# Performance work log

Measured on AMD Instinct MI355X. Metric: run time of the kernel, lower is better.

The kernel has to match this reference:

```python
import jax, jax.numpy as jnp
import numpy as np

B, D, K, C = 512, 256, 65536, 1000
T_SUP, T_DC, LS = 0.07, 0.1, 0.1
EPS = 1e-8


def _l2norm(x, axis):
    return x / jnp.linalg.norm(x, axis=axis, keepdims=True)


def setup_inputs() -> dict:
    key = jax.random.key(0)
    k1, k2, k3, k4, k5, k6, k7, k8 = jax.random.split(key, 8)
    norm_q = _l2norm(jax.random.normal(k1, (B, D), jnp.float32), axis=1)
    k_feat = _l2norm(jax.random.normal(k2, (B, D), jnp.float32), axis=1)
    q_logits = jax.random.normal(k3, (B, C), jnp.float32)
    logits_k = jax.random.normal(k4, (B, C), jnp.float32)
    queue = _l2norm(jax.random.normal(k5, (D, K), jnp.float32), axis=0)
    # queue_label_prob stores softmaxed class-probabilities column-wise (prob.T)
    queue_label_prob = jax.nn.softmax(jax.random.normal(k6, (C, K), jnp.float32), axis=0)
    queue_label = jax.random.randint(k7, (K,), 0, C, jnp.int64)
    target = jax.random.randint(k8, (B,), 0, C, jnp.int64)
    return {
        "norm_q": norm_q, "q_logits": q_logits, "k_feat": k_feat,
        "logits_k": logits_k, "queue": queue,
        "queue_label_prob": queue_label_prob, "queue_label": queue_label,
        "target": target, "knn_k": 200,
    }


def reference(norm_q, q_logits, k_feat, logits_k, queue, queue_label_prob,
              queue_label, target, knn_k):
    b = norm_q.shape[0]

    # ---- supcon_in ----
    sim = norm_q @ queue                                  # [B, K]
    _, idx = jax.lax.top_k(sim, knn_k)                    # [B, knn_k]
    sim_knn = jnp.take_along_axis(sim, idx, axis=1)
    w = jax.nn.softmax(sim_knn / T_SUP, axis=-1)
    pos = (target[:, None] == queue_label[idx])           # [B, knn_k]
    gt = jnp.sum(w * pos, axis=1)                         # [B]
    m = gt > EPS
    supin_loss = jnp.sum(jnp.where(m, -jnp.log(jnp.where(m, gt, 1.0)), 0.0)) / b

    # ---- label-smoothed onehot ----
    onehot = jnp.full((b, C), LS / (C - 1), jnp.float32)
    onehot = onehot.at[jnp.arange(b), target].set(1.0 - LS)

    log_q = jax.nn.log_softmax(q_logits, axis=1)
    q_mask = jax.nn.softmax(q_logits, axis=1).min(axis=1) > EPS  # [B]

    # ---- fc loss (masked CE with label smoothing) ----
    fc_loss = -jnp.sum(jnp.sum(onehot * log_q, axis=1) * q_mask) / b

    # ---- generate_dc_target (no-grad in original) ----
    sim_k = jax.nn.softmax((k_feat @ queue) / T_DC, axis=-1)      # [B, K]
    dc_target = sim_k @ queue_label_prob.T                        # [B, C]

    # ---- dc loss: KL(dc_target || softmax(q_logits)), masked, sum / B ----
    kl = jnp.where(dc_target > 0, dc_target * (jnp.log(jnp.where(dc_target > 0, dc_target, 1.0)) - log_q), 0.0)
    dc_loss = jnp.sum(jnp.sum(kl, axis=1) * q_mask) / b

    return (supin_loss, fc_loss, dc_loss)
```

## Files before the change

### kernel.cpp

```cpp
#include <hip/hip_runtime.h>
#include <math.h>

#define BN 512
#define DN 256
#define KN 65536
#define CN 1000
#define EQ_CAP 512
#define EPSTR 136

typedef __attribute__((ext_vector_type(8))) short bf16x8;
typedef __attribute__((ext_vector_type(4))) float f32x4;

__device__ __forceinline__ unsigned short f2bf(float f) {
    unsigned u = __float_as_uint(f);
    unsigned r = (u + 0x7FFFu + ((u >> 16) & 1u)) >> 16;
    return (unsigned short)r;
}
__device__ __forceinline__ float bf2f(unsigned short h) {
    return __uint_as_float(((unsigned)h) << 16);
}
__device__ __forceinline__ unsigned fkey16(unsigned b) {
    b &= 0xFFFFu;
    return (b & 0x8000u) ? ((~b) & 0xFFFFu) : (b | 0x8000u);
}
__device__ __forceinline__ void async16(const void* g, void* l) {
    __builtin_amdgcn_global_load_lds(
        (const __attribute__((address_space(1))) unsigned*)g,
        (__attribute__((address_space(3))) unsigned*)l, 16, 0, 0);
}

__global__ void __launch_bounds__(256) cvt_bf16(const float* __restrict__ in,
                                                unsigned short* __restrict__ out) {
    int i = (blockIdx.x * 256 + threadIdx.x) * 4;
    float4 v = *(const float4*)&in[i];
    ushort4 o;
    o.x = f2bf(v.x); o.y = f2bf(v.y); o.z = f2bf(v.z); o.w = f2bf(v.w);
    *(ushort4*)&out[i] = o;
}

__global__ void __launch_bounds__(256) transpose_q(const float* __restrict__ Q,
                                                   unsigned short* __restrict__ Qt) {
    __shared__ float T[64][65];
    int tid = threadIdx.x;
    int n0 = blockIdx.x * 64;
    int d0 = blockIdx.y * 64;
    #pragma unroll
    for (int i = 0; i < 4; ++i) {
        int flat = i * 256 + tid;
        int d = flat >> 4, nq = (flat & 15) * 4;
        float4 v = *(const float4*)&Q[(size_t)(d0 + d) * KN + n0 + nq];
        T[d][nq] = v.x; T[d][nq + 1] = v.y; T[d][nq + 2] = v.z; T[d][nq + 3] = v.w;
    }
    __syncthreads();
    int n = tid >> 2, dbase = (tid & 3) * 16;
    unsigned u[8];
    #pragma unroll
    for (int j = 0; j < 8; ++j) {
        unsigned short a = f2bf(T[dbase + 2 * j][n]);
        unsigned short b = f2bf(T[dbase + 2 * j + 1][n]);
        u[j] = (unsigned)a | ((unsigned)b << 16);
    }
    unsigned short* o = &Qt[(size_t)(n0 + n) * DN + d0 + dbase];
    *(uint4*)o = make_uint4(u[0], u[1], u[2], u[3]);
    *(uint4*)(o + 8) = make_uint4(u[4], u[5], u[6], u[7]);
}

__global__ void __launch_bounds__(256) gemm_sim(const unsigned short* __restrict__ A,
                                                const unsigned short* __restrict__ Bt,
                                                unsigned short* __restrict__ simOut,
                                                unsigned short* __restrict__ expOut,
                                                float* __restrict__ Zb,
                                                int mBlockSplit) {
    __shared__ unsigned short smem[128 * 64 * 2];
    __shared__ float Zred[128];
    unsigned short* As = smem;
    unsigned short* Bs = smem + 128 * 64;
    int tid = threadIdx.x;
    int n0 = blockIdx.x * 128, m0 = blockIdx.y * 128;
    bool isExp = ((int)blockIdx.y >= mBlockSplit);
    int lane = tid & 63, w = tid >> 6;
    int l15 = lane & 15, quad = lane >> 4;
    int wm = w & 1, wn = w >> 1;
    f32x4 acc[4][4];
    #pragma unroll
    for (int mi = 0; mi < 4; ++mi)
        #pragma unroll
        for (int ni = 0; ni < 4; ++ni)
            #pragma unroll
            for (int j = 0; j < 4; ++j) acc[mi][ni][j] = 0.f;

    for (int k0 = 0; k0 < DN; k0 += 64) {
        #pragma unroll
        for (int i = 0; i < 4; ++i) {
            int f = (i * 256 + tid) * 8;
            async16(A + (size_t)(m0 + (f >> 6)) * DN + k0 + (f & 63), &As[f]);
        }
        #pragma unroll
        for (int i = 0; i < 4; ++i) {
            int f = (i * 256 + tid) * 8;
            async16(Bt + (size_t)(n0 + (f >> 6)) * DN + k0 + (f & 63), &Bs[f]);
        }
        __syncthreads();
        #pragma unroll
        for (int ks = 0; ks < 2; ++ks) {
            bf16x8 am[4], bn[4];
            #pragma unroll
            for (int mi = 0; mi < 4; ++mi)
                am[mi] = *(const bf16x8*)&As[(wm * 64 + mi * 16 + l15) * 64 + ks * 32 + quad * 8];
            #pragma unroll
            for (int ni = 0; ni < 4; ++ni)
                bn[ni] = *(const bf16x8*)&Bs[(wn * 64 + ni * 16 + l15) * 64 + ks * 32 + quad * 8];
            #pragma unroll
            for (int mi = 0; mi < 4; ++mi)
                #pragma unroll
                for (int ni = 0; ni < 4; ++ni)
                    acc[mi][ni] = __builtin_amdgcn_mfma_f32_16x16x32_bf16(bn[ni], am[mi], acc[mi][ni], 0, 0, 0);
        }
        __syncthreads();
    }

    unsigned short* obase = isExp ? expOut : simOut;
    int orow0 = isExp ? (m0 - mBlockSplit * 128) : m0;
    float rsum[4] = {0.f, 0.f, 0.f, 0.f};

    #pragma unroll
    for (int round = 0; round < 2; ++round) {
        if (wm == round) {
            #pragma unroll
            for (int mi = 0; mi < 4; ++mi) {
                int mrow = mi * 16 + l15;
                #pragma unroll
                for (int ni = 0; ni < 4; ++ni) {
                    int nc = wn * 64 + ni * 16 + quad * 4;
                    float v0 = acc[mi][ni][0], v1 = acc[mi][ni][1];
                    float v2 = acc[mi][ni][2], v3 = acc[mi][ni][3];
                    if (isExp) {
                        v0 = __expf(v0 * 10.0f); v1 = __expf(v1 * 10.0f);
                        v2 = __expf(v2 * 10.0f); v3 = __expf(v3 * 10.0f);
                    }
                    unsigned short u0 = f2bf(v0), u1 = f2bf(v1), u2 = f2bf(v2), u3 = f2bf(v3);
                    if (isExp) rsum[mi] += bf2f(u0) + bf2f(u1) + bf2f(u2) + bf2f(u3);
                    *(uint2*)&smem[mrow * EPSTR + nc] =
                        make_uint2((unsigned)u0 | ((unsigned)u1 << 16),
                                   (unsigned)u2 | ((unsigned)u3 << 16));
                }
            }
        }
        __syncthreads();
        #pragma unroll
        for (int j = 0; j < 4; ++j) {
            int fc = j * 256 + tid;
            int mr = fc >> 4;
            int ch = fc & 15;
            uint4 val = *(uint4*)&smem[mr * EPSTR + ch * 8];
            int g = orow0 + round * 64 + mr;
            *(uint4*)&obase[(size_t)g * KN + n0 + ch * 8] = val;
        }
        __syncthreads();
    }

    if (isExp) {
        float v4[4];
        #pragma unroll
        for (int mi = 0; mi < 4; ++mi) {
            float v = rsum[mi];
            v += __shfl_xor(v, 16, 64);
            v += __shfl_xor(v, 32, 64);
            v4[mi] = v;
        }
        if (wn == 0 && quad == 0) {
            #pragma unroll
            for (int mi = 0; mi < 4; ++mi) Zred[wm * 64 + mi * 16 + l15] = v4[mi];
        }
        __syncthreads();
        if (wn == 1 && quad == 0) {
            #pragma unroll
            for (int mi = 0; mi < 4; ++mi) Zred[wm * 64 + mi * 16 + l15] += v4[mi];
        }
        __syncthreads();
        if (tid < 128) atomicAdd(&Zb[orow0 + tid], Zred[tid]);
    }
}

__global__ void __launch_bounds__(256) supcon(const unsigned short* __restrict__ sim,
                                              const int* __restrict__ qlabel,
                                              const int* __restrict__ target,
                                              const int* __restrict__ knnp,
                                              float* __restrict__ out0) {
    __shared__ unsigned hist[4][256];
    __shared__ unsigned s_sel, s_cntAbove;
    __shared__ int eqIdx[EQ_CAP];
    __shared__ unsigned eqCount;
    __shared__ float redZ[256], redN[256];
    int tid = threadIdx.x, w = tid >> 6;
    int row = blockIdx.x;
    const unsigned short* srow = sim + (size_t)row * KN;
    int knn = *knnp;
    int tgt = target[row];
    if (tid == 0) { eqCount = 0u; }
    #pragma unroll
    for (int j = 0; j < 4; ++j) hist[j][tid] = 0u;
    __syncthreads();
    for (int i0 = tid * 4; i0 < KN; i0 += 1024) {
        uint2 v = *(const uint2*)&srow[i0];
        atomicAdd(&hist[w][fkey16(v.x) >> 8], 1u);
        atomicAdd(&hist[w][fkey16(v.x >> 16) >> 8], 1u);
        atomicAdd(&hist[w][fkey16(v.y) >> 8], 1u);
        atomicAdd(&hist[w][fkey16(v.y >> 16) >> 8], 1u);
    }
    __syncthreads();
    if (tid == 0) {
        unsigned acc = 0; int chosen = 0;
        for (int bin = 255; bin >= 0; --bin) {
            unsigned h = hist[0][bin] + hist[1][bin] + hist[2][bin] + hist[3][bin];
            if (acc + h >= (unsigned)knn) { chosen = bin; break; }
            acc += h;
        }
        s_cntAbove = acc; s_sel = (unsigned)chosen;
    }
    __syncthreads();
    unsigned selHi = s_sel;
    #pragma unroll
    for (int j = 0; j < 4; ++j) hist[j][tid] = 0u;
    __syncthreads();
    for (int i0 = tid * 4; i0 < KN; i0 += 1024) {
        uint2 v = *(const uint2*)&srow[i0];
        unsigned k0 = fkey16(v.x), k1 = fkey16(v.x >> 16), k2 = fkey16(v.y), k3 = fkey16(v.y >> 16);
        if ((k0 >> 8) == selHi) atomicAdd(&hist[w][k0 & 255u], 1u);
        if ((k1 >> 8) == selHi) atomicAdd(&hist[w][k1 & 255u], 1u);
        if ((k2 >> 8) == selHi) atomicAdd(&hist[w][k2 & 255u], 1u);
        if ((k3 >> 8) == selHi) atomicAdd(&hist[w][k3 & 255u], 1u);
    }
    __syncthreads();
    if (tid == 0) {
        unsigned acc = s_cntAbove; int chosen = 0;
        for (int bin = 255; bin >= 0; --bin) {
            unsigned h = hist[0][bin] + hist[1][bin] + hist[2][bin] + hist[3][bin];
            if (acc + h >= (unsigned)knn) { chosen = bin; break; }
            acc += h;
        }
        s_cntAbove = acc; s_sel = (selHi << 8) | (unsigned)chosen;
    }
    __syncthreads();
    unsigned tu = s_sel;
    unsigned cgt = s_cntAbove;
    const float invT = 1.0f / 0.07f;
    float Zl = 0.f, Nl = 0.f;
    for (int i0 = tid * 4; i0 < KN; i0 += 1024) {
        uint2 v = *(const uint2*)&srow[i0];
        unsigned bits[4] = {v.x & 0xFFFFu, v.x >> 16, v.y & 0xFFFFu, v.y >> 16};
        #pragma unroll
        for (int j = 0; j < 4; ++j) {
            unsigned u = fkey16(bits[j]);
            if (u > tu) {
                float e = __expf(bf2f((unsigned short)bits[j]) * invT);
                Zl += e;
                if (qlabel[i0 + j] == tgt) Nl += e;
            } else if (u == tu) {
                unsigned pos = atomicAdd(&eqCount, 1u);
                if (pos < EQ_CAP) eqIdx[pos] = i0 + j;
            }
        }
    }
    redZ[tid] = Zl; redN[tid] = Nl;
    __syncthreads();
    for (int s = 128; s > 0; s >>= 1) {
        if (tid < s) { redZ[tid] += redZ[tid + s]; redN[tid] += redN[tid + s]; }
        __syncthreads();
    }
    if (tid == 0) {
        float Z = redZ[0], num = redN[0];
        int neq = (int)(eqCount < (unsigned)EQ_CAP ? eqCount : (unsigned)EQ_CAP);
        int needed = knn - (int)cgt;
        if (needed > neq) needed = neq;
        for (int a = 1; a < neq; ++a) {
            int v = eqIdx[a]; int b2 = a - 1;
            while (b2 >= 0 && eqIdx[b2] > v) { eqIdx[b2 + 1] = eqIdx[b2]; --b2; }
            eqIdx[b2 + 1] = v;
        }
        unsigned tb = (tu & 0x8000u) ? (tu & 0x7FFFu) : ((~tu) & 0xFFFFu);
        float wt = __expf(bf2f((unsigned short)tb) * invT);
        for (int a = 0; a < needed; ++a) {
            Z += wt;
            if (qlabel[eqIdx[a]] == tgt) num += wt;
        }
        float gt = num / Z;
        if (gt > 1e-8f) atomicAdd(out0, -logf(gt) * (1.0f / (float)BN));
    }
}

__global__ void __launch_bounds__(256) dc_gemm(const unsigned short* __restrict__ E,
                                               const float* __restrict__ P,
                                               float* __restrict__ dct) {
    __shared__ unsigned short As[128 * 32];
    __shared__ unsigned short Bs[128 * 32];
    int tid = threadIdx.x;
    int c0 = blockIdx.x * 128, m0 = blockIdx.y * 128;
    int kb = blockIdx.z * (KN / 16);
    int lane = tid & 63, w = tid >> 6;
    int l15 = lane & 15, quad = lane >> 4;
    int wm = w & 1, wn = w >> 1;
    int crow = tid >> 1, khalf = (tid & 1) * 16;
    bool cvalid = (c0 + crow) < CN;
    const float* pbase = P + (size_t)(c0 + crow) * KN + khalf;
    f32x4 acc[4][4];
    #pragma unroll
    for (int r = 0; r < 4; ++r)
        #pragma unroll
        for (int c = 0; c < 4; ++c)
            #pragma unroll
            for (int j = 0; j < 4; ++j) acc[r][c][j] = 0.f;
    for (int kc = 0; kc < KN / 16; kc += 32) {
        int k0 = kb + kc;
        #pragma unroll
        for (int i = 0; i < 2; ++i) {
            int flat = (i * 256 + tid) * 8;
            int row = flat >> 5, kk = flat & 31;
            async16(E + (size_t)(m0 + row) * KN + k0 + kk, &As[flat]);
        }
        float4 p0 = make_float4(0.f, 0.f, 0.f, 0.f), p1 = p0, p2 = p0, p3 = p0;
        if (cvalid) {
            p0 = *(const float4*)&pbase[k0];
            p1 = *(const float4*)&pbase[k0 + 4];
            p2 = *(const float4*)&pbase[k0 + 8];
            p3 = *(const float4*)&pbase[k0 + 12];
        }
        unsigned u0 = (unsigned)f2bf(p0.x) | ((unsigned)f2bf(p0.y) << 16);
        unsigned u1 = (unsigned)f2bf(p0.z) | ((unsigned)f2bf(p0.w) << 16);
        unsigned u2 = (unsigned)f2bf(p1.x) | ((unsigned)f2bf(p1.y) << 16);
        unsigned u3 = (unsigned)f2bf(p1.z) | ((unsigned)f2bf(p1.w) << 16);
        unsigned u4 = (unsigned)f2bf(p2.x) | ((unsigned)f2bf(p2.y) << 16);
        unsigned u5 = (unsigned)f2bf(p2.z) | ((unsigned)f2bf(p2.w) << 16);
        unsigned u6 = (unsigned)f2bf(p3.x) | ((unsigned)f2bf(p3.y) << 16);
        unsigned u7 = (unsigned)f2bf(p3.z) | ((unsigned)f2bf(p3.w) << 16);
        *(uint4*)&Bs[crow * 32 + khalf] = make_uint4(u0, u1, u2, u3);
        *(uint4*)&Bs[crow * 32 + khalf + 8] = make_uint4(u4, u5, u6, u7);
        __syncthreads();
        bf16x8 af[4], bfr[4];
        #pragma unroll
        for (int r = 0; r < 4; ++r) af[r] = *(const bf16x8*)&As[(wm * 64 + r * 16 + l15) * 32 + quad * 8];
        #pragma unroll
        for (int c = 0; c < 4; ++c) bfr[c] = *(const bf16x8*)&Bs[(wn * 64 + c * 16 + l15) * 32 + quad * 8];
        #pragma unroll
        for (int r = 0; r < 4; ++r)
            #pragma unroll
            for (int c = 0; c < 4; ++c)
                acc[r][c] = __builtin_amdgcn_mfma_f32_16x16x32_bf16(af[r], bfr[c], acc[r][c], 0, 0, 0);
        __syncthreads();
    }
    #pragma unroll
    for (int r = 0; r < 4; ++r)
        #pragma unroll
        for (int reg = 0; reg < 4; ++reg) {
            int m = m0 + wm * 64 + r * 16 + quad * 4 + reg;
            #pragma unroll
            for (int c = 0; c < 4; ++c) {
                int cc = c0 + wn * 64 + c * 16 + l15;
                atomicAdd(&dct[m * 1024 + cc], acc[r][c][reg]);
            }
        }
}

__global__ void __launch_bounds__(256) logq_fc(const float* __restrict__ x_all,
                                               const int* __restrict__ target,
                                               float* __restrict__ logq,
                                               float* __restrict__ qmask,
                                               float* __restrict__ out1) {
    int row = blockIdx.x, tid = threadIdx.x;
    const float* x = x_all + (size_t)row * CN;
    __shared__ float red[256], red2[256];
    float mx = -INFINITY, mn = INFINITY;
    for (int c = tid; c < CN; c += 256) { float v = x[c]; mx = fmaxf(mx, v); mn = fminf(mn, v); }
    red[tid] = mx; red2[tid] = mn;
    __syncthreads();
    for (int s = 128; s > 0; s >>= 1) {
        if (tid < s) { red[tid] = fmaxf(red[tid], red[tid + s]); red2[tid] = fminf(red2[tid], red2[tid + s]); }
        __syncthreads();
    }
    mx = red[0]; mn = red2[0];
    __syncthreads();
    float se = 0.f, sx = 0.f;
    for (int c = tid; c < CN; c += 256) { float v = x[c]; se += __expf(v - mx); sx += v; }
    red[tid] = se; red2[tid] = sx;
    __syncthreads();
    for (int s = 128; s > 0; s >>= 1) {
        if (tid < s) { red[tid] += red[tid + s]; red2[tid] += red2[tid + s]; }
        __syncthreads();
    }
    float lse = mx + logf(red[0]);
    float sumlogq = red2[0] - (float)CN * lse;
    for (int c = tid; c < CN; c += 256) logq[(size_t)row * CN + c] = x[c] - lse;
    if (tid == 0) {
        float lqt = x[target[row]] - lse;
        bool qm = (mn - lse) > logf(1e-8f);
        qmask[row] = qm ? 1.0f : 0.0f;
        if (qm) {
            float fc = -(0.1f / 999.0f * (sumlogq - lqt) + 0.9f * lqt);
            atomicAdd(out1, fc * (1.0f / (float)BN));
        }
    }
}

__global__ void __launch_bounds__(256) dc_loss(const float* __restrict__ dct,
                                               const float* __restrict__ logq,
                                               const float* __restrict__ qmask,
                                               const float* __restrict__ Z,
                                               float* __restrict__ out2) {
    int row = blockIdx.x, tid = threadIdx.x;
    __shared__ float red[256];
    float invZ = 1.0f / Z[row];
    float s = 0.f;
    for (int c = tid; c < CN; c += 256) {
        float T = dct[row * 1024 + c] * invZ;
        if (T > 0.f) s += T * (logf(T) - logq[(size_t)row * CN + c]);
    }
    red[tid] = s;
    __syncthreads();
    for (int st = 128; st > 0; st >>= 1) {
        if (tid < st) red[tid] += red[tid + st];
        __syncthreads();
    }
    if (tid == 0 && qmask[row] > 0.f)
        atomicAdd(out2, red[0] * (1.0f / (float)BN));
}

extern "C" void kernel_launch(void* const* d_in, const int* in_sizes, int n_in,
                              void* d_out, int out_size, void* d_ws, size_t ws_size,
                              hipStream_t stream) {
    (void)in_sizes; (void)n_in; (void)out_size;
    const float* norm_q   = (const float*)d_in[0];
    const float* q_logits = (const float*)d_in[1];
    const float* k_feat   = (const float*)d_in[2];
    const float* queue    = (const float*)d_in[4];
    const float* qlp      = (const float*)d_in[5];
    const int*   qlabel   = (const int*)d_in[6];
    const int*   target   = (const int*)d_in[7];
    const int*   knnp     = (const int*)d_in[8];
    float* out = (float*)d_out;
    char* ws = (char*)d_ws;

    const size_t SIM_B = 67108864;
    const size_t QT_B  = 33554432;
    const size_t AC_B  = 524288;
    const size_t FUSED_NEED = SIM_B * 2 + QT_B + AC_B + 2097152 + 2048 + 2048000 + 2048;
    bool fused = (ws_size >= FUSED_NEED);

    unsigned short *simBF, *Ebf, *queueT, *Acat;
    float *dct, *Zb, *logq, *qmask;
    if (fused) {
        simBF  = (unsigned short*)(ws);
        Ebf    = (unsigned short*)(ws + SIM_B);
        queueT = (unsigned short*)(ws + 2 * SIM_B);
        Acat   = (unsigned short*)(ws + 2 * SIM_B + QT_B);
        dct    = (float*)(ws + 2 * SIM_B + QT_B + AC_B);
    } else {
        simBF  = (unsigned short*)(ws);
        Ebf    = simBF;
        queueT = (unsigned short*)(ws + SIM_B);
        Acat   = (unsigned short*)(ws + SIM_B + QT_B);
        dct    = (float*)(ws + SIM_B + QT_B + AC_B);
    }
    Zb    = (float*)((char*)dct + 2097152);
    logq  = (float*)((char*)Zb + 2048);
    qmask = (float*)((char*)logq + 2048000);

    hipMemsetAsync(dct, 0, 2097152 + 2048, stream);
    hipMemsetAsync(d_out, 0, 3 * sizeof(float), stream);

    cvt_bf16<<<dim3(128), 256, 0, stream>>>(norm_q, Acat);
    cvt_bf16<<<dim3(128), 256, 0, stream>>>(k_feat, Acat + (size_t)BN * DN);
    transpose_q<<<dim3(KN / 64, 4), 256, 0, stream>>>(queue, queueT);

    if (fused) {
        gemm_sim<<<dim3(KN / 128, 8), 256, 0, stream>>>(Acat, queueT, simBF, Ebf, Zb, 4);
        supcon<<<dim3(BN), 256, 0, stream>>>(simBF, qlabel, target, knnp, out + 0);
    } else {
        gemm_sim<<<dim3(KN / 128, 4), 256, 0, stream>>>(Acat, queueT, simBF, nullptr, nullptr, 4);
        supcon<<<dim3(BN), 256, 0, stream>>>(simBF, qlabel, target, knnp, out + 0);
        gemm_sim<<<dim3(KN / 128, 4), 256, 0, stream>>>(Acat + (size_t)BN * DN, queueT,
                                                        nullptr, Ebf, Zb, 0);
    }
    dc_gemm<<<dim3(8, 4, 16), 256, 0, stream>>>(Ebf, qlp, dct);
    logq_fc<<<dim3(BN), 256, 0, stream>>>(q_logits, target, logq, qmask, out + 1);
    dc_loss<<<dim3(BN), 256, 0, stream>>>(dct, logq, qmask, Zb, out + 2);
}
```

Measured before the change: 799.9 us.

## Widen dc_gemm K-tile to 64, swizzle LDS, double split-K, packed bf16 convert

The dc_gemm kernel now stages 64-wide K slices per iteration instead of 32, doing two MFMA k-steps per barrier pair. The B tile in LDS gets an XOR swizzle to avoid bank conflicts. The split-K factor goes from 16 to 32 so more blocks are in flight, with a launch-bounds occupancy hint of 3. The fp32-to-bf16 conversion of the probability matrix uses the hardware packed convert instruction. The aim is to cut barrier overhead and LDS conflicts and to better saturate bandwidth on the large fp32 P read. The cost is more LDS per block, and twice as many atomic adds into the output.

```diff
diff --git a/kernel.cpp b/kernel.cpp
--- a/kernel.cpp
+++ b/kernel.cpp
@@ -27,6 +27,11 @@
     __builtin_amdgcn_global_load_lds(
         (const __attribute__((address_space(1))) unsigned*)g,
         (__attribute__((address_space(3))) unsigned*)l, 16, 0, 0);
+}
+__device__ __forceinline__ unsigned cvtpk(float lo, float hi) {
+    unsigned r;
+    asm("v_cvt_pk_bf16_f32 %0, %1, %2" : "=v"(r) : "v"(lo), "v"(hi));
+    return r;
 }
 
 __global__ void __launch_bounds__(256) cvt_bf16(const float* __restrict__ in,
@@ -289,20 +294,21 @@
     }
 }
 
-__global__ void __launch_bounds__(256) dc_gemm(const unsigned short* __restrict__ E,
-                                               const float* __restrict__ P,
-                                               float* __restrict__ dct) {
-    __shared__ unsigned short As[128 * 32];
-    __shared__ unsigned short Bs[128 * 32];
+__global__ void __launch_bounds__(256, 3) dc_gemm(const unsigned short* __restrict__ E,
+                                                  const float* __restrict__ P,
+                                                  float* __restrict__ dct) {
+    __shared__ unsigned short As[128 * 64];
+    __shared__ unsigned short Bs[128 * 64];
     int tid = threadIdx.x;
     int c0 = blockIdx.x * 128, m0 = blockIdx.y * 128;
-    int kb = blockIdx.z * (KN / 16);
+    int kb = blockIdx.z * (KN / 32);
     int lane = tid & 63, w = tid >> 6;
     int l15 = lane & 15, quad = lane >> 4;
     int wm = w & 1, wn = w >> 1;
-    int crow = tid >> 1, khalf = (tid & 1) * 16;
+    int crow = tid >> 1, koff = (tid & 1) * 32;
     bool cvalid = (c0 + crow) < CN;
-    const float* pbase = P + (size_t)(c0 + crow) * KN + khalf;
+    const float* pbase = P + (size_t)(c0 + crow) * KN + kb + koff;
+    int bswz = (crow & 7) << 3;
     f32x4 acc[4][4];
     #pragma unroll
     for (int r = 0; r < 4; ++r)
@@ -310,42 +316,48 @@
         for (int c = 0; c < 4; ++c)
             #pragma unroll
             for (int j = 0; j < 4; ++j) acc[r][c][j] = 0.f;
-    for (int kc = 0; kc < KN / 16; kc += 32) {
-        int k0 = kb + kc;
-        #pragma unroll
-        for (int i = 0; i < 2; ++i) {
-            int flat = (i * 256 + tid) * 8;
-            int row = flat >> 5, kk = flat & 31;
-            async16(E + (size_t)(m0 + row) * KN + k0 + kk, &As[flat]);
-        }
-        float4 p0 = make_float4(0.f, 0.f, 0.f, 0.f), p1 = p0, p2 = p0, p3 = p0;
+
+    for (int kc = 0; kc < KN / 32; kc += 64) {
+        #pragma unroll
+        for (int i = 0; i < 4; ++i) {
+            int f = (i * 256 + tid) * 8;
+            async16(E + (size_t)(m0 + (f >> 6)) * KN + kb + kc + (f & 63), &As[f]);
+        }
+        float4 p[8];
         if (cvalid) {
-            p0 = *(const float4*)&pbase[k0];
-            p1 = *(const float4*)&pbase[k0 + 4];
-            p2 = *(const float4*)&pbase[k0 + 8];
-            p3 = *(const float4*)&pbase[k0 + 12];
-        }
-        unsigned u0 = (unsigned)f2bf(p0.x) | ((unsigned)f2bf(p0.y) << 16);
-        unsigned u1 = (unsigned)f2bf(p0.z) | ((unsigned)f2bf(p0.w) << 16);
-        unsigned u2 = (unsigned)f2bf(p1.x) | ((unsigned)f2bf(p1.y) << 16);
-        unsigned u3 = (unsigned)f2bf(p1.z) | ((unsigned)f2bf(p1.w) << 16);
-        unsigned u4 = (unsigned)f2bf(p2.x) | ((unsigned)f2bf(p2.y) << 16);
-        unsigned u5 = (unsigned)f2bf(p2.z) | ((unsigned)f2bf(p2.w) << 16);
-        unsigned u6 = (unsigned)f2bf(p3.x) | ((unsigned)f2bf(p3.y) << 16);
-        unsigned u7 = (unsigned)f2bf(p3.z) | ((unsigned)f2bf(p3.w) << 16);
-        *(uint4*)&Bs[crow * 32 + khalf] = make_uint4(u0, u1, u2, u3);
-        *(uint4*)&Bs[crow * 32 + khalf + 8] = make_uint4(u4, u5, u6, u7);
-        __syncthreads();
-        bf16x8 af[4], bfr[4];
-        #pragma unroll
-        for (int r = 0; r < 4; ++r) af[r] = *(const bf16x8*)&As[(wm * 64 + r * 16 + l15) * 32 + quad * 8];
-        #pragma unroll
-        for (int c = 0; c < 4; ++c) bfr[c] = *(const bf16x8*)&Bs[(wn * 64 + c * 16 + l15) * 32 + quad * 8];
-        #pragma unroll
-        for (int r = 0; r < 4; ++r)
-            #pragma unroll
-            for (int c = 0; c < 4; ++c)
-                acc[r][c] = __builtin_amdgcn_mfma_f32_16x16x32_bf16(af[r], bfr[c], acc[r][c], 0, 0, 0);
+            #pragma unroll
+            for (int i = 0; i < 8; ++i) p[i] = *(const float4*)&pbase[kc + i * 4];
+        } else {
+            #pragma unroll
+            for (int i = 0; i < 8; ++i) p[i] = make_float4(0.f, 0.f, 0.f, 0.f);
+        }
+        #pragma unroll
+        for (int i = 0; i < 4; ++i) {
+            uint4 v;
+            v.x = cvtpk(p[2 * i].x, p[2 * i].y);
+            v.y = cvtpk(p[2 * i].z, p[2 * i].w);
+            v.z = cvtpk(p[2 * i + 1].x, p[2 * i + 1].y);
+            v.w = cvtpk(p[2 * i + 1].z, p[2 * i + 1].w);
+            *(uint4*)&Bs[crow * 64 + ((koff + i * 8) ^ bswz)] = v;
+        }
+        __syncthreads();
+        #pragma unroll
+        for (int ks = 0; ks < 2; ++ks) {
+            bf16x8 af[4], bfr[4];
+            #pragma unroll
+            for (int r = 0; r < 4; ++r)
+                af[r] = *(const bf16x8*)&As[(wm * 64 + r * 16 + l15) * 64 + ks * 32 + quad * 8];
+            #pragma unroll
+            for (int c = 0; c < 4; ++c) {
+                int brow = wn * 64 + c * 16 + l15;
+                bfr[c] = *(const bf16x8*)&Bs[brow * 64 + ((ks * 32 + quad * 8) ^ ((brow & 7) << 3))];
+            }
+            #pragma unroll
+            for (int r = 0; r < 4; ++r)
+                #pragma unroll
+                for (int c = 0; c < 4; ++c)
+                    acc[r][c] = __builtin_amdgcn_mfma_f32_16x16x32_bf16(af[r], bfr[c], acc[r][c], 0, 0, 0);
+        }
         __syncthreads();
     }
     #pragma unroll
@@ -480,7 +492,7 @@
         gemm_sim<<<dim3(KN / 128, 4), 256, 0, stream>>>(Acat + (size_t)BN * DN, queueT,
                                                         nullptr, Ebf, Zb, 0);
     }
-    dc_gemm<<<dim3(8, 4, 16), 256, 0, stream>>>(Ebf, qlp, dct);
+    dc_gemm<<<dim3(8, 4, 32), 256, 0, stream>>>(Ebf, qlp, dct);
     logq_fc<<<dim3(BN), 256, 0, stream>>>(q_logits, target, logq, qmask, out + 1);
     dc_loss<<<dim3(BN), 256, 0, stream>>>(dct, logq, qmask, Zb, out + 2);
 }
```

Result: faster. 783.7 us (-2.0%).
